# Performance work log

Hardware: AMD Instinct MI355X
Metric: run time of the kernel (lower is better)

Reference implementation:

```python
import jax, jax.numpy as jnp
import numpy as np

EMB = 2048
NQH = 16          # num_q_heads
G = 4             # group_size
NKV = NQH // G    # 4 kv heads
HD = EMB // NQH   # 128 head_dim
B, S = 2, 2048


def setup_inputs() -> dict:
    key = jax.random.key(0)
    ks = jax.random.split(key, 6)
    scale = 1.0 / np.sqrt(EMB)
    x = jax.random.normal(ks[0], (B, S, EMB), dtype=jnp.float32)
    attn_mask = jnp.zeros((B, S), dtype=bool)  # unused placeholder
    # torch Linear weights: (out_features, in_features)
    Wq = jax.random.normal(ks[1], (EMB, EMB), dtype=jnp.float32) * scale
    Wk = jax.random.normal(ks[2], (EMB // G, EMB), dtype=jnp.float32) * scale
    Wv = jax.random.normal(ks[3], (EMB // G, EMB), dtype=jnp.float32) * scale
    Wo = jax.random.normal(ks[4], (EMB, EMB), dtype=jnp.float32) * scale
    return {"x": x, "attn_mask": attn_mask, "is_causal": 1,
            "Wq": Wq, "Wk": Wk, "Wv": Wv, "Wo": Wo}


def reference(x, attn_mask, is_causal, Wq, Wk, Wv, Wo):
    b, n, _ = x.shape
    q = x @ Wq.T                      # (b, n, EMB)
    k = x @ Wk.T                      # (b, n, EMB//G)
    v = x @ Wv.T                      # (b, n, EMB//G)
    # q: b n (h_full d) -> b h_full n d, then (h g) split with h=NKV outer
    q = q.reshape(b, n, NQH, HD).transpose(0, 2, 1, 3)      # (b, NQH, n, d)
    q = q.reshape(b, NKV, G, n, HD).transpose(0, 2, 1, 3, 4)  # (b, g, h, n, d)
    k = k.reshape(b, n, NKV, HD).transpose(0, 2, 1, 3)      # (b, h, s, d)
    v = v.reshape(b, n, NKV, HD).transpose(0, 2, 1, 3)      # (b, h, s, d)
    attn = jnp.einsum('bghnd,bhsd->bghns', q, k) / np.sqrt(HD)
    scores = jax.nn.softmax(attn, axis=-1)  # dropout p=0.0 -> identity
    out = jnp.einsum('bghns,bhsd->bghnd', scores, v)        # (b, g, h, n, d)
    # b g h n d -> b n (h g) d -> b n (h g d)
    out = out.transpose(0, 3, 2, 1, 4).reshape(b, n, EMB)
    y = out @ Wo.T
    return y
```

## Files before the change

kernel.cpp:

```cpp
#include <hip/hip_runtime.h>
#include <stdint.h>


typedef short s8v __attribute__((ext_vector_type(8)));
typedef float f4  __attribute__((ext_vector_type(4)));
typedef unsigned short u16;

#define GLD_LDS(g, l) __builtin_amdgcn_global_load_lds(                     \
    (const __attribute__((address_space(1))) void*)(g),                     \
    (__attribute__((address_space(3))) void*)(l), 16, 0, 0)

__device__ __forceinline__ u16 f2bf(float f) {
    union { float f; uint32_t u; } v; v.f = f;
    uint32_t u = v.u;
    return (u16)((u + 0x7fffu + ((u >> 16) & 1u)) >> 16);
}

__device__ __forceinline__ float fexp2(float x) {
#if __has_builtin(__builtin_amdgcn_exp2f)
    return __builtin_amdgcn_exp2f(x);
#else
    return exp2f(x);
#endif
}

__global__ void cvt_all(const float* __restrict__ x,  const float* __restrict__ wq,
                        const float* __restrict__ wk, const float* __restrict__ wv,
                        const float* __restrict__ wo_,
                        u16* __restrict__ xb, u16* __restrict__ wqkv,
                        u16* __restrict__ wob)
{
    int i = blockIdx.x * blockDim.x + threadIdx.x;
    const float4* s; ushort4* d; int so, dofs;
    if (i < 2097152)      { s = (const float4*)x;   d = (ushort4*)xb;   so = i;           dofs = so; }
    else if (i < 3145728) { s = (const float4*)wq;  d = (ushort4*)wqkv; so = i - 2097152; dofs = so; }
    else if (i < 3407872) { s = (const float4*)wk;  d = (ushort4*)wqkv; so = i - 3145728; dofs = so + 1048576; }
    else if (i < 3670016) { s = (const float4*)wv;  d = (ushort4*)wqkv; so = i - 3407872; dofs = so + 1310720; }
    else                  { s = (const float4*)wo_; d = (ushort4*)wob;  so = i - 3670016; dofs = so; }
    float4 v = s[so];
    ushort4 o;
    o.x = f2bf(v.x); o.y = f2bf(v.y); o.z = f2bf(v.z); o.w = f2bf(v.w);
    d[dofs] = o;
}

template<int MODE>
__global__ __launch_bounds__(256, 3)
void gemm_bt(const u16* __restrict__ A, const u16* __restrict__ Bm,
             int M, int N, int K,
             u16* __restrict__ qkOut, u16* __restrict__ vtOut,
             float* __restrict__ fOut)
{
    __shared__ __attribute__((aligned(16))) u16 As[128 * 32];
    __shared__ __attribute__((aligned(16))) u16 Bs[128 * 32];

    const int tid  = threadIdx.x;
    const int wave = tid >> 6, lane = tid & 63;
    const int quad = lane >> 4, l16 = lane & 15;
    const int wr = wave >> 1, wc = wave & 1;

    int bx, by;
    {
        const int nwgx = gridDim.x;
        const int nwg  = nwgx * gridDim.y;
        const int flat = blockIdx.y * nwgx + blockIdx.x;
        const int nflat = (flat & 7) * (nwg >> 3) + (flat >> 3);
        bx = nflat % nwgx; by = nflat / nwgx;
    }
    const int m0 = by * 128, n0 = bx * 128;

    const int rowC = lane >> 2;
    const int slot = lane & 3;

    f4 acc[4][4] = {};

    for (int k0 = 0; k0 < K; k0 += 32) {
        #pragma unroll
        for (int i = 0; i < 4; i++) {
            const int c  = wave + i * 4;
            const int ch = c & 7;
            const int row = ch * 16 + rowC;
            const int glog = slot ^ (row & 3);
            const u16* gsrc = (c < 8)
                ? (A  + (size_t)(m0 + row) * K + k0 + glog * 8)
                : (Bm + (size_t)(n0 + row) * K + k0 + glog * 8);
            u16* lbase = (c < 8) ? (As + ch * 512) : (Bs + ch * 512);
            GLD_LDS(gsrc, lbase);
        }
        __syncthreads();

        s8v af[4], bfr[4];
        #pragma unroll
        for (int t = 0; t < 4; t++) {
            int row = wr * 64 + t * 16 + l16;
            af[t] = *(const s8v*)(As + row * 32 + ((quad ^ (row & 3)) * 8));
        }
        #pragma unroll
        for (int u = 0; u < 4; u++) {
            int row = wc * 64 + u * 16 + l16;
            bfr[u] = *(const s8v*)(Bs + row * 32 + ((quad ^ (row & 3)) * 8));
        }
        #pragma unroll
        for (int t = 0; t < 4; t++)
            #pragma unroll
            for (int u = 0; u < 4; u++)
                acc[t][u] = __builtin_amdgcn_mfma_f32_16x16x32_bf16(
                    af[t], bfr[u], acc[t][u], 0, 0, 0);
        __syncthreads();
    }

    if (MODE == 0) {
        if (n0 < 2560) {
            const float qs = (n0 < 2048)
                ? (0.08838834764831845f * 1.4426950408889634f) : 1.0f;
            #pragma unroll
            for (int t = 0; t < 4; t++) {
                int gm0 = m0 + wr * 64 + t * 16 + quad * 4;
                #pragma unroll
                for (int u = 0; u < 4; u++) {
                    int gn = n0 + wc * 64 + u * 16 + l16;
                    #pragma unroll
                    for (int r = 0; r < 4; r++)
                        qkOut[(size_t)(gm0 + r) * 2560 + gn] = f2bf(acc[t][u][r] * qs);
                }
            }
        } else {
            #pragma unroll
            for (int t = 0; t < 4; t++) {
                int gm0 = m0 + wr * 64 + t * 16 + quad * 4;
                int bb = gm0 >> 11, s = gm0 & 2047;
                #pragma unroll
                for (int u = 0; u < 4; u++) {
                    int gn = n0 + wc * 64 + u * 16 + l16;
                    int dd = gn - 2560;
                    ushort4 pk;
                    pk.x = f2bf(acc[t][u][0]); pk.y = f2bf(acc[t][u][1]);
                    pk.z = f2bf(acc[t][u][2]); pk.w = f2bf(acc[t][u][3]);
                    *(ushort4*)(vtOut +
                        ((size_t)(bb * 4 + (dd >> 7)) * 128 + (dd & 127)) * 2048 + s) = pk;
                }
            }
        }
    } else {
        #pragma unroll
        for (int t = 0; t < 4; t++) {
            int gm0 = m0 + wr * 64 + t * 16 + quad * 4;
            #pragma unroll
            for (int u = 0; u < 4; u++) {
                int gn = n0 + wc * 64 + u * 16 + l16;
                #pragma unroll
                for (int r = 0; r < 4; r++)
                    fOut[(size_t)(gm0 + r) * N + gn] = acc[t][u][r];
            }
        }
    }
}

__global__ __launch_bounds__(256, 1)
void attn_kernel(const u16* __restrict__ qk, const u16* __restrict__ vt,
                 u16* __restrict__ ao)
{
    __shared__ __attribute__((aligned(16))) u16 Kb[2][64 * 128];
    __shared__ __attribute__((aligned(16))) u16 Vb[2][128 * 64];
    __shared__ __attribute__((aligned(16))) u16 Ps[4][64 * 72];

    const int tid  = threadIdx.x;
    const int wave = tid >> 6, lane = tid & 63;
    const int quad = lane >> 4, l16 = lane & 15;
    const int bh = blockIdx.x;
    const int b = bh >> 2, h = bh & 3;
    const int hq = h * 4 + wave;
    const int qs0 = blockIdx.y * 64;

    s8v aq[4][4];
    #pragma unroll
    for (int mt = 0; mt < 4; mt++) {
        const u16* qrow = qk + (size_t)(b * 2048 + qs0 + mt * 16 + l16) * 2560
                             + hq * 128 + quad * 8;
        #pragma unroll
        for (int c4 = 0; c4 < 4; c4++) aq[mt][c4] = *(const s8v*)(qrow + c4 * 32);
    }

    s8v ones;
    #pragma unroll
    for (int j = 0; j < 8; j++) ones[j] = (short)0x3F80;

    f4 o[4][9] = {};

    const u16* kbase = qk + (size_t)(b * 2048) * 2560 + 2048 + h * 128;
    const u16* vbase = vt + (size_t)bh * 128 * 2048;
    u16* Pw = &Ps[wave][0];

    int bkb[4], bvb[2];
    #pragma unroll
    for (int c4 = 0; c4 < 4; c4++)
        bkb[c4] = l16 * 128 + (((c4 * 4 + quad) ^ (l16 & 7)) * 8);
    #pragma unroll
    for (int kc = 0; kc < 2; kc++)
        bvb[kc] = l16 * 64 + (((kc * 4 + quad) ^ (l16 & 7)) * 8);
    const int apb = l16 * 72 + quad * 8;
    const int pwb = quad * 4 * 72 + l16;

#define STAGE(CUR, S) {                                                       \
        _Pragma("unroll")                                                     \
        for (int i = 0; i < 4; i++) {                                         \
            const int c = wave + i * 4;                                       \
            int kr = c * 4 + (lane >> 4);                                     \
            int ksw = (lane & 15) ^ (kr & 7);                                 \
            GLD_LDS(kbase + (size_t)((S) + kr) * 2560 + ksw * 8,              \
                    &Kb[CUR][c * 512]);                                       \
            int vd = c * 8 + (lane >> 3);                                     \
            int vsw = (lane & 7) ^ (vd & 7);                                  \
            GLD_LDS(vbase + (size_t)vd * 2048 + (S) + vsw * 8,                \
                    &Vb[CUR][c * 512]);                                       \
        } }

#define STEP(CUR, S) {                                                        \
        __syncthreads();    \
        if ((S) + 64 < 2048) STAGE((CUR) ^ 1, (S) + 64);                      \
        s8v bk[4][4];                                                         \
        _Pragma("unroll")                                                     \
        for (int c4 = 0; c4 < 4; c4++)                                        \
            _Pragma("unroll")                                                 \
            for (int cg = 0; cg < 4; cg++)                                    \
                bk[c4][cg] = *(const s8v*)(&Kb[CUR][bkb[c4] + cg * 2048]);    \
        _Pragma("unroll")                                                     \
        for (int mt = 0; mt < 4; mt++) {                                      \
            f4 sc[4] = {};                                                    \
            _Pragma("unroll")                                                 \
            for (int c4 = 0; c4 < 4; c4++)                                    \
                _Pragma("unroll")                                             \
                for (int cg = 0; cg < 4; cg++)                                \
                    sc[cg] = __builtin_amdgcn_mfma_f32_16x16x32_bf16(         \
                        aq[mt][c4], bk[c4][cg], sc[cg], 0, 0, 0);             \
              \
            _Pragma("unroll")                                                 \
            for (int cg = 0; cg < 4; cg++)                                    \
                _Pragma("unroll")                                             \
                for (int r = 0; r < 4; r++)                                   \
                    Pw[pwb + mt * 1152 + r * 72 + cg * 16] =                  \
                        (u16)(__float_as_uint(fexp2(sc[cg][r])) >> 16);       \
        }                                                                     \
        s8v ap[4][2];                                                         \
        _Pragma("unroll")                                                     \
        for (int mt = 0; mt < 4; mt++)                                        \
            _Pragma("unroll")                                                 \
            for (int kc = 0; kc < 2; kc++)                                    \
                ap[mt][kc] = *(const s8v*)(Pw + apb + mt * 1152 + kc * 32);   \
        _Pragma("unroll")                                                     \
        for (int ch = 0; ch < 8; ch++) {                                      \
            s8v bv0 = *(const s8v*)(&Vb[CUR][bvb[0] + ch * 1024]);            \
            s8v bv1 = *(const s8v*)(&Vb[CUR][bvb[1] + ch * 1024]);            \
            _Pragma("unroll")                                                 \
            for (int mt = 0; mt < 4; mt++) {                                  \
                o[mt][ch] = __builtin_amdgcn_mfma_f32_16x16x32_bf16(          \
                    ap[mt][0], bv0, o[mt][ch], 0, 0, 0);                      \
                o[mt][ch] = __builtin_amdgcn_mfma_f32_16x16x32_bf16(          \
                    ap[mt][1], bv1, o[mt][ch], 0, 0, 0);                      \
            }                                                                 \
        }                                                                     \
        _Pragma("unroll")                                                     \
        for (int mt = 0; mt < 4; mt++) {                                      \
            o[mt][8] = __builtin_amdgcn_mfma_f32_16x16x32_bf16(               \
                ap[mt][0], ones, o[mt][8], 0, 0, 0);                          \
            o[mt][8] = __builtin_amdgcn_mfma_f32_16x16x32_bf16(               \
                ap[mt][1], ones, o[mt][8], 0, 0, 0);                          \
        } }

    STAGE(0, 0);
    for (int s0 = 0; s0 < 2048; s0 += 128) {
        STEP(0, s0);
        STEP(1, s0 + 64);
    }
#undef STEP
#undef STAGE

    #pragma unroll
    for (int mt = 0; mt < 4; mt++)
        #pragma unroll
        for (int r = 0; r < 4; r++) {
            float inv = 1.f / o[mt][8][r];
            int gm = b * 2048 + qs0 + mt * 16 + quad * 4 + r;
            #pragma unroll
            for (int ch = 0; ch < 8; ch++)
                ao[(size_t)gm * 2048 + hq * 128 + ch * 16 + l16] =
                    f2bf(o[mt][ch][r] * inv);
        }
}

extern "C" void kernel_launch(void* const* d_in, const int* in_sizes, int n_in,
                              void* d_out, int out_size, void* d_ws, size_t ws_size,
                              hipStream_t stream)
{
    const float* x  = (const float*)d_in[0];
    const float* Wq = (const float*)d_in[3];
    const float* Wk = (const float*)d_in[4];
    const float* Wv = (const float*)d_in[5];
    const float* Wo = (const float*)d_in[6];

    char* ws = (char*)d_ws;
    u16* xb   = (u16*)(ws);
    u16* wqkv = (u16*)(ws + 16777216);
    u16* wo   = (u16*)(ws + 29360128);
    u16* qkb  = (u16*)(ws + 37748736);
    u16* vtb  = (u16*)(ws + 58720256);
    u16* ao   = (u16*)(ws + 62914560);
    if (ws_size < 79691776u) return;

    cvt_all<<<18432, 256, 0, stream>>>(x, Wq, Wk, Wv, Wo, xb, wqkv, wo);

    gemm_bt<0><<<dim3(24, 32), 256, 0, stream>>>(xb, wqkv, 4096, 3072, 2048,
                                                 qkb, vtb, nullptr);
    attn_kernel<<<dim3(8, 32), 256, 0, stream>>>(qkb, vtb, ao);
    gemm_bt<1><<<dim3(16, 32), 256, 0, stream>>>(ao, wo, 4096, 2048, 2048,
                                                 nullptr, nullptr, (float*)d_out);
}
```

Baseline: 309.2 us.

## Replace 128x128 GEMM with 256x256-tile double-buffered pipelined GEMM

Both projection GEMMs move from a 128x128 tile, 256-thread, single-buffered kernel to a 256x256 tile with 512 threads and K-step 64. LDS is double-buffered, global-to-LDS loads for later K-steps are interleaved between MFMA quarter-blocks, and waits use explicit vmcnt counts and raw barriers with raised wave priority during MFMA. The aim is to hide global load latency and raise arithmetic intensity per tile. The cost is far fewer workgroups (192 and 128 on a 256-CU part), which leaves some CUs idle, plus more registers per thread and more LDS.

Result: slower. 316.3 us (+2.3%).

```diff
diff --git a/kernel.cpp b/kernel.cpp
--- a/kernel.cpp
+++ b/kernel.cpp
@@ -44,19 +44,18 @@
 }
 
 template<int MODE>
-__global__ __launch_bounds__(256, 3)
-void gemm_bt(const u16* __restrict__ A, const u16* __restrict__ Bm,
+__global__ __launch_bounds__(512, 2)
+void gemm256(const u16* __restrict__ A, const u16* __restrict__ Bm,
              int M, int N, int K,
              u16* __restrict__ qkOut, u16* __restrict__ vtOut,
              float* __restrict__ fOut)
 {
-    __shared__ __attribute__((aligned(16))) u16 As[128 * 32];
-    __shared__ __attribute__((aligned(16))) u16 Bs[128 * 32];
+    __shared__ __attribute__((aligned(16))) u16 lds[2][2][2][8192];
 
     const int tid  = threadIdx.x;
-    const int wave = tid >> 6, lane = tid & 63;
-    const int quad = lane >> 4, l16 = lane & 15;
-    const int wr = wave >> 1, wc = wave & 1;
+    const int lane = tid & 63, quad = lane >> 4, l16 = lane & 15;
+    const int wave = tid >> 6;
+    const int wr = wave >> 2, wc = wave & 3;
 
     int bx, by;
     {
@@ -66,75 +65,124 @@
         const int nflat = (flat & 7) * (nwg >> 3) + (flat >> 3);
         bx = nflat % nwgx; by = nflat / nwgx;
     }
-    const int m0 = by * 128, n0 = bx * 128;
-
-    const int rowC = lane >> 2;
-    const int slot = lane & 3;
-
-    f4 acc[4][4] = {};
-
-    for (int k0 = 0; k0 < K; k0 += 32) {
-        #pragma unroll
-        for (int i = 0; i < 4; i++) {
-            const int c  = wave + i * 4;
-            const int ch = c & 7;
-            const int row = ch * 16 + rowC;
-            const int glog = slot ^ (row & 3);
-            const u16* gsrc = (c < 8)
-                ? (A  + (size_t)(m0 + row) * K + k0 + glog * 8)
-                : (Bm + (size_t)(n0 + row) * K + k0 + glog * 8);
-            u16* lbase = (c < 8) ? (As + ch * 512) : (Bs + ch * 512);
-            GLD_LDS(gsrc, lbase);
-        }
-        __syncthreads();
-
-        s8v af[4], bfr[4];
-        #pragma unroll
-        for (int t = 0; t < 4; t++) {
-            int row = wr * 64 + t * 16 + l16;
-            af[t] = *(const s8v*)(As + row * 32 + ((quad ^ (row & 3)) * 8));
-        }
-        #pragma unroll
-        for (int u = 0; u < 4; u++) {
-            int row = wc * 64 + u * 16 + l16;
-            bfr[u] = *(const s8v*)(Bs + row * 32 + ((quad ^ (row & 3)) * 8));
-        }
-        #pragma unroll
-        for (int t = 0; t < 4; t++)
-            #pragma unroll
-            for (int u = 0; u < 4; u++)
-                acc[t][u] = __builtin_amdgcn_mfma_f32_16x16x32_bf16(
-                    af[t], bfr[u], acc[t][u], 0, 0, 0);
-        __syncthreads();
-    }
+    const int m0 = by * 256, n0 = bx * 256;
+    const int NT = K >> 6;
+
+    f4 acc[8][4] = {};
+
+#define VMC6() asm volatile("s_waitcnt vmcnt(6)" ::: "memory")
+#define VMC0() asm volatile("s_waitcnt vmcnt(0)" ::: "memory")
+#define BAR()  __builtin_amdgcn_s_barrier()
+
+#define STG(bf, op, h, t) if ((t) < NT) {                                   \
+        const u16* gb = (op) ? Bm : A;                                      \
+        const int rb = ((op) ? n0 : m0) + (h) * 128;                        \
+        _Pragma("unroll")                                                   \
+        for (int j = 0; j < 2; j++) {                                       \
+            int s_ = j * 512 + tid;                                         \
+            int r_ = s_ >> 3, cc = s_ & 7;                                  \
+            GLD_LDS(gb + (size_t)(rb + r_) * K + (t) * 64                   \
+                       + ((cc ^ (r_ & 7)) << 3),                            \
+                    &lds[bf][op][h][(j * 512 + (tid & ~63)) * 8]);          \
+        } }
+
+#define RD_A(bf, qm, ar) {                                                  \
+        _Pragma("unroll")                                                   \
+        for (int f = 0; f < 4; f++) {                                       \
+            int r_ = (qm) * 64 + f * 16 + l16;                              \
+            _Pragma("unroll")                                               \
+            for (int kc = 0; kc < 2; kc++)                                  \
+                ar[f][kc] = *(const s8v*)(&lds[bf][0][wr]                   \
+                    [r_ * 64 + (((kc * 4 + quad) ^ (r_ & 7)) << 3)]);       \
+        } }
+
+#define RD_B(bf, qn, br) {                                                  \
+        _Pragma("unroll")                                                   \
+        for (int f = 0; f < 2; f++) {                                       \
+            int r_ = (wc & 1) * 64 + ((qn) * 2 + f) * 16 + l16;             \
+            _Pragma("unroll")                                               \
+            for (int kc = 0; kc < 2; kc++)                                  \
+                br[f][kc] = *(const s8v*)(&lds[bf][1][wc >> 1]              \
+                    [r_ * 64 + (((kc * 4 + quad) ^ (r_ & 7)) << 3)]);       \
+        } }
+
+#define MM(qm, qn, ar, br) {                                                \
+        __builtin_amdgcn_s_setprio(1);                                      \
+        _Pragma("unroll")                                                   \
+        for (int f = 0; f < 4; f++)                                         \
+            _Pragma("unroll")                                               \
+            for (int g = 0; g < 2; g++) {                                   \
+                acc[(qm)*4+f][(qn)*2+g] = __builtin_amdgcn_mfma_f32_16x16x32_bf16( \
+                    ar[f][0], br[g][0], acc[(qm)*4+f][(qn)*2+g], 0, 0, 0);  \
+                acc[(qm)*4+f][(qn)*2+g] = __builtin_amdgcn_mfma_f32_16x16x32_bf16( \
+                    ar[f][1], br[g][1], acc[(qm)*4+f][(qn)*2+g], 0, 0, 0);  \
+            }                                                               \
+        __builtin_amdgcn_s_setprio(0); }
+
+    STG(0,1,0,0); STG(0,1,1,0); STG(0,0,0,0); STG(0,0,1,0);
+    STG(1,1,0,1); STG(1,1,1,1); STG(1,0,0,1);
+    VMC6(); BAR();
+
+    for (int T = 0; T < NT; T += 2) {
+        const bool more = (T + 2 < NT);
+        s8v a0[4][2], a1[4][2], b0[2][2], b1[2][2];
+        RD_A(0,0,a0); RD_B(0,0,b0);
+        STG(1,0,1,T+1);
+        BAR(); MM(0,0,a0,b0); BAR();
+        RD_B(0,1,b1);
+        BAR(); MM(0,1,a0,b1); BAR();
+        RD_A(0,1,a1);
+        STG(0,1,0,T+2);
+        BAR(); MM(1,0,a1,b0); BAR();
+        STG(0,1,1,T+2); STG(0,0,0,T+2);
+        BAR(); MM(1,1,a1,b1);
+        if (more) { VMC6(); } else { VMC0(); }
+        BAR();
+        RD_A(1,0,a0); RD_B(1,0,b0);
+        STG(0,0,1,T+2);
+        BAR(); MM(0,0,a0,b0); BAR();
+        RD_B(1,1,b1);
+        BAR(); MM(0,1,a0,b1); BAR();
+        RD_A(1,1,a1);
+        STG(1,1,0,T+3);
+        BAR(); MM(1,0,a1,b0); BAR();
+        STG(1,1,1,T+3); STG(1,0,0,T+3);
+        BAR(); MM(1,1,a1,b1);
+        if (more) { VMC6(); } else { VMC0(); }
+        BAR();
+    }
+#undef STG
+#undef RD_A
+#undef RD_B
+#undef MM
 
     if (MODE == 0) {
         if (n0 < 2560) {
             const float qs = (n0 < 2048)
                 ? (0.08838834764831845f * 1.4426950408889634f) : 1.0f;
             #pragma unroll
-            for (int t = 0; t < 4; t++) {
-                int gm0 = m0 + wr * 64 + t * 16 + quad * 4;
+            for (int mi = 0; mi < 8; mi++) {
+                int gm0 = m0 + wr * 128 + mi * 16 + quad * 4;
                 #pragma unroll
-                for (int u = 0; u < 4; u++) {
-                    int gn = n0 + wc * 64 + u * 16 + l16;
+                for (int ni = 0; ni < 4; ni++) {
+                    int gn = n0 + wc * 64 + ni * 16 + l16;
                     #pragma unroll
                     for (int r = 0; r < 4; r++)
-                        qkOut[(size_t)(gm0 + r) * 2560 + gn] = f2bf(acc[t][u][r] * qs);
+                        qkOut[(size_t)(gm0 + r) * 2560 + gn] = f2bf(acc[mi][ni][r] * qs);
                 }
             }
         } else {
             #pragma unroll
-            for (int t = 0; t < 4; t++) {
-                int gm0 = m0 + wr * 64 + t * 16 + quad * 4;
+            for (int mi = 0; mi < 8; mi++) {
+                int gm0 = m0 + wr * 128 + mi * 16 + quad * 4;
                 int bb = gm0 >> 11, s = gm0 & 2047;
                 #pragma unroll
-                for (int u = 0; u < 4; u++) {
-                    int gn = n0 + wc * 64 + u * 16 + l16;
+                for (int ni = 0; ni < 4; ni++) {
+                    int gn = n0 + wc * 64 + ni * 16 + l16;
                     int dd = gn - 2560;
                     ushort4 pk;
-                    pk.x = f2bf(acc[t][u][0]); pk.y = f2bf(acc[t][u][1]);
-                    pk.z = f2bf(acc[t][u][2]); pk.w = f2bf(acc[t][u][3]);
+                    pk.x = f2bf(acc[mi][ni][0]); pk.y = f2bf(acc[mi][ni][1]);
+                    pk.z = f2bf(acc[mi][ni][2]); pk.w = f2bf(acc[mi][ni][3]);
                     *(ushort4*)(vtOut +
                         ((size_t)(bb * 4 + (dd >> 7)) * 128 + (dd & 127)) * 2048 + s) = pk;
                 }
@@ -142,17 +190,20 @@
         }
     } else {
         #pragma unroll
-        for (int t = 0; t < 4; t++) {
-            int gm0 = m0 + wr * 64 + t * 16 + quad * 4;
+        for (int mi = 0; mi < 8; mi++) {
+            int gm0 = m0 + wr * 128 + mi * 16 + quad * 4;
             #pragma unroll
-            for (int u = 0; u < 4; u++) {
-                int gn = n0 + wc * 64 + u * 16 + l16;
+            for (int ni = 0; ni < 4; ni++) {
+                int gn = n0 + wc * 64 + ni * 16 + l16;
                 #pragma unroll
                 for (int r = 0; r < 4; r++)
-                    fOut[(size_t)(gm0 + r) * N + gn] = acc[t][u][r];
+                    fOut[(size_t)(gm0 + r) * N + gn] = acc[mi][ni][r];
             }
         }
     }
+#undef VMC6
+#undef VMC0
+#undef BAR
 }
 
 __global__ __launch_bounds__(256, 1)
@@ -215,7 +266,7 @@
         } }
 
 #define STEP(CUR, S) {                                                        \
-        __syncthreads();    \
+        __syncthreads();                                                      \
         if ((S) + 64 < 2048) STAGE((CUR) ^ 1, (S) + 64);                      \
         s8v bk[4][4];                                                         \
         _Pragma("unroll")                                                     \
@@ -232,7 +283,6 @@
                 for (int cg = 0; cg < 4; cg++)                                \
                     sc[cg] = __builtin_amdgcn_mfma_f32_16x16x32_bf16(         \
                         aq[mt][c4], bk[c4][cg], sc[cg], 0, 0, 0);             \
-              \
             _Pragma("unroll")                                                 \
             for (int cg = 0; cg < 4; cg++)                                    \
                 _Pragma("unroll")                                             \
@@ -308,9 +358,9 @@
 
     cvt_all<<<18432, 256, 0, stream>>>(x, Wq, Wk, Wv, Wo, xb, wqkv, wo);
 
-    gemm_bt<0><<<dim3(24, 32), 256, 0, stream>>>(xb, wqkv, 4096, 3072, 2048,
+    gemm256<0><<<dim3(12, 16), 512, 0, stream>>>(xb, wqkv, 4096, 3072, 2048,
                                                  qkb, vtb, nullptr);
     attn_kernel<<<dim3(8, 32), 256, 0, stream>>>(qkb, vtb, ao);
-    gemm_bt<1><<<dim3(16, 32), 256, 0, stream>>>(ao, wo, 4096, 2048, 2048,
-                                                 nullptr, nullptr, (float*)d_out);
-}
+    gemm256<1><<<dim3(8, 16), 512, 0, stream>>>(ao, wo, 4096, 2048, 2048,
+                                                nullptr, nullptr, (float*)d_out);
+}
```
